# Kernel optimization log

Hardware: AMD Instinct MI355X
Metric: run time of the kernel (lower is better)

The kernel has to match this reference:

```python
import jax, jax.numpy as jnp
import numpy as np

B, H, W = 4, 180, 180
C_L, C_C, C_OUT = 128, 128, 256
CH_ALL = 2 * (C_L + C_C)        # 512
CH_HID = CH_ALL // 3            # 170


def setup_inputs() -> dict:
    key = jax.random.key(0)
    ks = jax.random.split(key, 12)
    N = 160000
    inp = {
        'lidar_features': jax.random.normal(ks[0], (N, C_L), dtype=jnp.float32),
        'img_bev': jax.random.normal(ks[1], (B, C_C, H, W), dtype=jnp.float32),
        'batch_idx': jnp.sort(jax.random.randint(ks[2], (N,), 0, B, dtype=jnp.int32)),
        'y_idx': jax.random.randint(ks[3], (N,), 0, H, dtype=jnp.int32),
        'x_idx': jax.random.randint(ks[4], (N,), 0, W, dtype=jnp.int32),
        # weights stored as [in, out] (x @ W), equivalent to torch Linear weight.T
        'Wl1': jax.random.normal(ks[5], (CH_ALL, CH_HID), dtype=jnp.float32) * 0.02,
        'Wl2': jax.random.normal(ks[6], (CH_HID, C_L), dtype=jnp.float32) * 0.02,
        'Wc1': jax.random.normal(ks[7], (CH_ALL, CH_HID), dtype=jnp.float32) * 0.02,
        'Wc2': jax.random.normal(ks[8], (CH_HID, C_C), dtype=jnp.float32) * 0.02,
        'Wf1': jax.random.normal(ks[9], (C_L + C_C, C_OUT), dtype=jnp.float32) * 0.02,
        'Wf2': jax.random.normal(ks[10], (C_OUT, C_OUT), dtype=jnp.float32) * 0.02,
    }
    return inp


def reference(lidar_features, img_bev, Wl1, Wl2, Wc1, Wc2, Wf1, Wf2,
              batch_idx, y_idx, x_idx):
    relu = jax.nn.relu
    spatial_size = H * W
    # flatten dense image BEV map: [B,C,H,W] -> [B*H*W, C]
    img_flat = jnp.transpose(img_bev, (0, 2, 3, 1)).reshape(B * H * W, C_C)
    # per-voxel flat row index (faithful to original incl. clamp to spatial_size-2)
    row = batch_idx * spatial_size + y_idx * W + x_idx
    row = jnp.clip(row, 0, spatial_size - 2)
    cam_feat = img_flat[row]                                  # [N, C_C] gather
    # per-batch segment min/max (ragged reduction)
    lmin = jax.ops.segment_min(lidar_features, batch_idx, num_segments=B)
    lmax = jax.ops.segment_max(lidar_features, batch_idx, num_segments=B)
    cmin = jax.ops.segment_min(cam_feat, batch_idx, num_segments=B)
    cmax = jax.ops.segment_max(cam_feat, batch_idx, num_segments=B)
    cat_mm = jnp.concatenate([lmin, lmax, cmin, cmax], axis=-1)   # [B, 512]
    att_l = jax.nn.sigmoid(relu(relu(cat_mm @ Wl1) @ Wl2))        # [B, C_L]
    att_c = jax.nn.sigmoid(relu(relu(cat_mm @ Wc1) @ Wc2))        # [B, C_C]
    gated_l = lidar_features * att_l[batch_idx]
    gated_c = cam_feat * att_c[batch_idx]
    fused = jnp.concatenate([gated_l, gated_c], axis=-1)          # [N, 256]
    out = relu(relu(fused @ Wf1) @ Wf2)                           # [N, 256]
    return out
```

## Files before the change

kernel.cpp:

```cpp
#include <hip/hip_runtime.h>
#include <math.h>

#define NB 4
#define HH 180
#define WWW 180
#define SPATIAL (HH*WWW)
#define CH_HID 170
#define CLAMP_ROW (SPATIAL-2)
#define SLAB 8192
#define CHUNKB 256

typedef short v8s __attribute__((ext_vector_type(8)));
typedef short v4s __attribute__((ext_vector_type(4)));
typedef float v4f __attribute__((ext_vector_type(4)));

__device__ __forceinline__ unsigned short f2bf(float f) {
    unsigned u = __float_as_uint(f);
    u += 0x7FFFu + ((u >> 16) & 1);
    return (unsigned short)(u >> 16);
}
__device__ __forceinline__ v4f vmin4(v4f a, v4f b) {
    v4f r; r[0]=fminf(a[0],b[0]); r[1]=fminf(a[1],b[1]); r[2]=fminf(a[2],b[2]); r[3]=fminf(a[3],b[3]); return r;
}
__device__ __forceinline__ v4f vmax4(v4f a, v4f b) {
    v4f r; r[0]=fmaxf(a[0],b[0]); r[1]=fmaxf(a[1],b[1]); r[2]=fmaxf(a[2],b[2]); r[3]=fmaxf(a[3],b[3]); return r;
}

__global__ void k_prep(const float* __restrict__ Wf1, const float* __restrict__ Wf2,
                       unsigned short* __restrict__ W1S, unsigned short* __restrict__ W2S) {
    const float* W = blockIdx.y ? Wf2 : Wf1;
    unsigned short* WS = blockIdx.y ? W2S : W1S;
    const int tid = threadIdx.x;
    const int frag = blockIdx.x * 4 + (tid >> 6);
    const int lane = tid & 63;
    const int nt = frag >> 3, ks = frag & 7;
    const int q = lane >> 4, ml = lane & 15;
    v8s pk;
    #pragma unroll
    for (int j = 0; j < 8; ++j)
        pk[j] = (short)f2bf(W[(ks*32 + q*8 + j)*256 + nt*16 + ml]);
    *(v8s*)&WS[(frag*64 + lane)*8] = pk;
}

__global__ void k_setup(const float* __restrict__ img, float* __restrict__ camT) {
    __shared__ float tile[32][33];
    int s0 = blockIdx.x * 32, c0 = blockIdx.y * 32;
    int lx = threadIdx.x & 31, ly = threadIdx.x >> 5;
    for (int i = 0; i < 4; ++i) {
        int s = s0 + lx;
        if (s < SPATIAL)
            tile[ly + i*8][lx] = img[(c0 + ly + i*8) * SPATIAL + s];
    }
    __syncthreads();
    for (int i = 0; i < 4; ++i) {
        int s = s0 + ly + i*8;
        if (s < SPATIAL)
            camT[s*128 + c0 + lx] = tile[lx][ly + i*8];
    }
}

__global__ __launch_bounds__(256)
void k_reduce(const float* __restrict__ lidar, const float* __restrict__ camT,
              const int* __restrict__ bidx, const int* __restrict__ yidx,
              const int* __restrict__ xidx,
              float* __restrict__ pA, float* __restrict__ pB, int N, int nblkA) {
    __shared__ __align__(16) char sm[32768];
    const int tid = threadIdx.x;

    if ((int)blockIdx.x < nblkA) {
        v4f (*red)[8][32] = (v4f(*)[8][32])sm;
        const int total = N * 32;
        const int beg = blockIdx.x * SLAB;
        const int end = min(beg + SLAB, total);
        const v4f pinf = {INFINITY, INFINITY, INFINITY, INFINITY};
        const v4f ninf = {-INFINITY, -INFINITY, -INFINITY, -INFINITY};
        v4f mn0 = pinf, mn1 = pinf, mn2 = pinf, mn3 = pinf;
        v4f mx0 = ninf, mx1 = ninf, mx2 = ninf, mx3 = ninf;

        #define ACCUM(vv, bb) do { \
            bool m0_ = ((bb) == 0), m1_ = ((bb) == 1), m2_ = ((bb) == 2), m3_ = ((bb) == 3); \
            mn0 = m0_ ? vmin4(mn0, (vv)) : mn0;  mx0 = m0_ ? vmax4(mx0, (vv)) : mx0; \
            mn1 = m1_ ? vmin4(mn1, (vv)) : mn1;  mx1 = m1_ ? vmax4(mx1, (vv)) : mx1; \
            mn2 = m2_ ? vmin4(mn2, (vv)) : mn2;  mx2 = m2_ ? vmax4(mx2, (vv)) : mx2; \
            mn3 = m3_ ? vmin4(mn3, (vv)) : mn3;  mx3 = m3_ ? vmax4(mx3, (vv)) : mx3; \
        } while (0)

        int i = beg + tid;
        for (; i + 768 < end; i += 1024) {
            v4f x0 = *(const v4f*)&lidar[(size_t)i * 4];
            v4f x1 = *(const v4f*)&lidar[(size_t)(i + 256) * 4];
            v4f x2 = *(const v4f*)&lidar[(size_t)(i + 512) * 4];
            v4f x3 = *(const v4f*)&lidar[(size_t)(i + 768) * 4];
            int b0 = bidx[i >> 5];
            int b1 = bidx[(i + 256) >> 5];
            int b2 = bidx[(i + 512) >> 5];
            int b3 = bidx[(i + 768) >> 5];
            ACCUM(x0, b0); ACCUM(x1, b1); ACCUM(x2, b2); ACCUM(x3, b3);
        }
        for (; i < end; i += 256) {
            v4f x = *(const v4f*)&lidar[(size_t)i * 4];
            int b = bidx[i >> 5];
            ACCUM(x, b);
        }
        #undef ACCUM

        const int sub = tid >> 5, cc = tid & 31;
        red[sub][0][cc] = mn0; red[sub][1][cc] = mx0;
        red[sub][2][cc] = mn1; red[sub][3][cc] = mx1;
        red[sub][4][cc] = mn2; red[sub][5][cc] = mx2;
        red[sub][6][cc] = mn3; red[sub][7][cc] = mx3;
        __syncthreads();
        const int acc = tid >> 5;
        const bool ismax = acc & 1;
        v4f r = red[0][acc][cc];
        #pragma unroll
        for (int s = 1; s < 8; ++s)
            r = ismax ? vmax4(r, red[s][acc][cc]) : vmin4(r, red[s][acc][cc]);
        *(v4f*)&pA[((size_t)blockIdx.x * 8 + acc) * 128 + cc * 4] = r;
    } else {
        int* srow = (int*)sm;
        v4f (*cred)[2][32] = (v4f(*)[2][32])(sm + 2048);
        const int blk = blockIdx.x - nblkA;
        const int vbeg = blk * CHUNKB;
        const int cnt = min(CHUNKB, N - vbeg);
        const bool active = (cnt > 0) && (bidx[vbeg] == 0);
        if (!active) {
            int a2 = tid >> 7, ch = tid & 127;
            pB[((size_t)blk * 2 + a2) * 128 + ch] = a2 ? -INFINITY : INFINITY;
            return;
        }
        if (tid < cnt) {
            int v = vbeg + tid;
            srow[tid] = (bidx[v] == 0) ? min(yidx[v] * WWW + xidx[v], CLAMP_ROW) : -1;
        }
        __syncthreads();
        const int c4 = (tid & 31) * 4;
        v4f mn = {INFINITY, INFINITY, INFINITY, INFINITY};
        v4f mx = {-INFINITY, -INFINITY, -INFINITY, -INFINITY};
        for (int idx = tid >> 5; idx < cnt; idx += 8) {
            int r = srow[idx];
            if (r >= 0) {
                v4f v = *(const v4f*)&camT[(size_t)r * 128 + c4];
                mn = vmin4(mn, v);
                mx = vmax4(mx, v);
            }
        }
        const int sub = tid >> 5, cc = tid & 31;
        cred[sub][0][cc] = mn;
        cred[sub][1][cc] = mx;
        __syncthreads();
        if (tid < 64) {
            const bool ismax = tid >= 32;
            v4f r = cred[0][ismax][cc];
            #pragma unroll
            for (int s = 1; s < 8; ++s)
                r = ismax ? vmax4(r, cred[s][ismax][cc]) : vmin4(r, cred[s][ismax][cc]);
            *(v4f*)&pB[((size_t)blk * 2 + (ismax ? 1 : 0)) * 128 + cc * 4] = r;
        }
    }
}

__global__ __launch_bounds__(256)
void k_fin(const float* __restrict__ pA, const float* __restrict__ pB,
           float* __restrict__ statsf, int nblkA, int nblkB) {
    __shared__ float red2[8][33];
    const int bx = blockIdx.x, tid = threadIdx.x;
    const int g = tid >> 5, l = tid & 31;
    const bool iscam = bx >= 32;
    const int acc = iscam ? ((bx - 32) >> 2) : (bx >> 2);
    const int quarter = bx & 3;
    const int ch = quarter * 32 + l;
    const int nrow = iscam ? nblkB : nblkA;
    const bool ismax = iscam ? (acc == 1) : ((acc & 1) != 0);
    const float* base = iscam ? (pB + acc * 128 + ch) : (pA + acc * 128 + ch);
    const size_t rstride = iscam ? 256 : 1024;

    float r = ismax ? -INFINITY : INFINITY;
    int row = g;
    for (; row + 24 < nrow; row += 32) {
        float a = base[(size_t)row * rstride];
        float b = base[(size_t)(row + 8) * rstride];
        float c = base[(size_t)(row + 16) * rstride];
        float d = base[(size_t)(row + 24) * rstride];
        if (ismax) r = fmaxf(fmaxf(r, a), fmaxf(fmaxf(b, c), d));
        else       r = fminf(fminf(r, a), fminf(fminf(b, c), d));
    }
    for (; row < nrow; row += 8) {
        float a = base[(size_t)row * rstride];
        r = ismax ? fmaxf(r, a) : fminf(r, a);
    }
    red2[g][l] = r;
    __syncthreads();
    if (tid < 32) {
        float v = red2[0][l];
        #pragma unroll
        for (int s = 1; s < 8; ++s)
            v = ismax ? fmaxf(v, red2[s][l]) : fminf(v, red2[s][l]);
        int off;
        if (iscam) off = 256 + acc * 128 + ch;
        else { int bb = acc >> 1; off = bb * 512 + (acc & 1) * 128 + ch; }
        statsf[off] = v;
    }
}

__global__ void k_mlp(const float* __restrict__ statsf, const float* __restrict__ camT,
                      const float* __restrict__ Wl1, const float* __restrict__ Wl2,
                      const float* __restrict__ Wc1, const float* __restrict__ Wc2,
                      float* __restrict__ att) {
    __shared__ float cat[512];
    __shared__ float hid[CH_HID];
    int b = blockIdx.x >> 1;
    int net = blockIdx.x & 1;
    const float* W1 = net ? Wc1 : Wl1;
    const float* W2 = net ? Wc2 : Wl2;
    int tid = threadIdx.x;
    for (int j = tid; j < 512; j += 256) {
        float x;
        if (j < 256 || b == 0) x = statsf[b * 512 + j];
        else                   x = camT[(size_t)CLAMP_ROW * 128 + (j & 127)];
        cat[j] = x;
    }
    __syncthreads();
    if (tid < CH_HID) {
        float s = 0.f;
        #pragma unroll 16
        for (int k = 0; k < 512; ++k) s += cat[k] * W1[k*CH_HID + tid];
        hid[tid] = fmaxf(s, 0.f);
    }
    __syncthreads();
    if (tid < 128) {
        float s = 0.f;
        #pragma unroll 10
        for (int k = 0; k < CH_HID; ++k) s += hid[k] * W2[k*128 + tid];
        s = fmaxf(s, 0.f);
        att[b*256 + net*128 + tid] = 1.f / (1.f + expf(-s));
    }
}

__global__ __launch_bounds__(256, 4)
void k_main(const float* __restrict__ lidar, const float* __restrict__ camT,
            const int* __restrict__ bidx, const int* __restrict__ yidx,
            const int* __restrict__ xidx, const float* __restrict__ att,
            const unsigned short* __restrict__ W1S, const unsigned short* __restrict__ W2S,
            float* __restrict__ out, int N) {
    __shared__ __align__(16) char smem[64 * 264 * 2];
    unsigned short (*sA)[264] = (unsigned short(*)[264])smem;
    float* sAf = (float*)smem;
    __shared__ int srow[64];
    __shared__ int sbb[64];
    const int tid = threadIdx.x;
    const int v0 = blockIdx.x * 64;

    if (tid < 64) {
        int v = v0 + tid;
        int b = 0, row = 0;
        if (v < N) {
            b = bidx[v];
            row = min(b*SPATIAL + yidx[v]*WWW + xidx[v], CLAMP_ROW);
        }
        sbb[tid] = b;
        srow[tid] = row;
    }
    const int c = (tid & 63) * 4;
    const bool cam = (c >= 128);
    v4f attv0 = *(const v4f*)&att[0*256 + c];
    v4f attv1 = *(const v4f*)&att[1*256 + c];
    v4f attv2 = *(const v4f*)&att[2*256 + c];
    v4f attv3 = *(const v4f*)&att[3*256 + c];
    __syncthreads();

    #pragma unroll
    for (int half = 0; half < 2; ++half) {
        v4f x[8]; int bm[8];
        #pragma unroll
        for (int j = 0; j < 8; ++j) {
            int m = (half*8 + j)*4 + (tid >> 6);
            int vc = min(v0 + m, N - 1);
            bm[j] = sbb[m];
            const float* src = cam ? &camT[(size_t)srow[m]*128 + (c - 128)]
                                   : &lidar[(size_t)vc*128 + c];
            x[j] = *(const v4f*)src;
        }
        #pragma unroll
        for (int j = 0; j < 8; ++j) {
            int m = (half*8 + j)*4 + (tid >> 6);
            int b = bm[j];
            v4f a = attv0;
            if (b == 1) a = attv1;
            if (b == 2) a = attv2;
            if (b == 3) a = attv3;
            v4f val = x[j] * a;
            v4s pk;
            #pragma unroll
            for (int jj = 0; jj < 4; ++jj) pk[jj] = (short)f2bf(val[jj]);
            *(v4s*)&sA[m][c] = pk;
        }
    }

    const int wave = tid >> 6;
    const int lane = tid & 63;
    const int ml = lane & 15;
    const int q = lane >> 4;

    v4f acc[4][4];
    for (int layer = 0; layer < 2; ++layer) {
        const unsigned short* WS = layer ? W2S : W1S;
        const v4f zz = {0.f, 0.f, 0.f, 0.f};
        for (int rt = 0; rt < 4; ++rt)
            for (int ct = 0; ct < 4; ++ct) acc[rt][ct] = zz;

        __syncthreads();
        #pragma unroll
        for (int ks = 0; ks < 8; ++ks) {
            v8s a[4];
            const int ka = ks*32 + q*8;
            #pragma unroll
            for (int rt = 0; rt < 4; ++rt)
                a[rt] = *(const v8s*)&sA[rt*16 + ml][ka];
            #pragma unroll
            for (int ct = 0; ct < 4; ++ct) {
                v8s bfr = *(const v8s*)&WS[(((wave*4 + ct)*8 + ks)*64 + lane)*8];
                #pragma unroll
                for (int rt = 0; rt < 4; ++rt)
                    acc[rt][ct] = __builtin_amdgcn_mfma_f32_16x16x32_bf16(
                        a[rt], bfr, acc[rt][ct], 0, 0, 0);
            }
        }
        __syncthreads();
        if (layer == 0) {
            for (int rt = 0; rt < 4; ++rt)
                for (int ct = 0; ct < 4; ++ct)
                    for (int r = 0; r < 4; ++r)
                        sA[rt*16 + q*4 + r][wave*64 + ct*16 + ml] =
                            f2bf(fmaxf(acc[rt][ct][r], 0.f));
        }
    }

    const int c4 = (tid & 63) * 4;
    #pragma unroll
    for (int p = 0; p < 2; ++p) {
        __syncthreads();
        #pragma unroll
        for (int rt = 2*p; rt < 2*p + 2; ++rt)
            for (int ct = 0; ct < 4; ++ct)
                for (int r = 0; r < 4; ++r)
                    sAf[((rt - 2*p)*16 + q*4 + r)*260 + wave*64 + ct*16 + ml] =
                        fmaxf(acc[rt][ct][r], 0.f);
        __syncthreads();
        #pragma unroll
        for (int i = 0; i < 8; ++i) {
            int rl = (tid >> 6) + i*4;
            int v = v0 + p*32 + rl;
            if (v < N)
                *(v4f*)&out[(size_t)v*256 + c4] = *(const v4f*)&sAf[rl*260 + c4];
        }
    }
}

extern "C" void kernel_launch(void* const* d_in, const int* in_sizes, int n_in,
                              void* d_out, int out_size, void* d_ws, size_t ws_size,
                              hipStream_t stream) {
    const float* lidar = (const float*)d_in[0];
    const float* img   = (const float*)d_in[1];
    const int*   bidx  = (const int*)d_in[2];
    const int*   yidx  = (const int*)d_in[3];
    const int*   xidx  = (const int*)d_in[4];
    const float* Wl1   = (const float*)d_in[5];
    const float* Wl2   = (const float*)d_in[6];
    const float* Wc1   = (const float*)d_in[7];
    const float* Wc2   = (const float*)d_in[8];
    const float* Wf1   = (const float*)d_in[9];
    const float* Wf2   = (const float*)d_in[10];
    float* out = (float*)d_out;
    const int N = in_sizes[0] / 128;

    float* statsf = (float*)d_ws;
    float* att = (float*)((char*)d_ws + 8192);
    unsigned short* W1S = (unsigned short*)((char*)d_ws + 16384);
    unsigned short* W2S = (unsigned short*)((char*)d_ws + 16384 + 131072);
    float* camT = (float*)((char*)d_ws + 16384 + 262144);

    const int nblkA = (N * 32 + SLAB - 1) / SLAB;
    const int nblkB = (N + CHUNKB - 1) / CHUNKB;
    const size_t pA_bytes = (size_t)nblkA * 8 * 128 * 4;
    const size_t pB_bytes = (size_t)nblkB * 2 * 128 * 4;
    const size_t pA_off = 16384 + 262144 + (size_t)SPATIAL * 128 * 4;
    float *pA, *pB;
    if (ws_size >= pA_off + pA_bytes + pB_bytes) {
        pA = (float*)((char*)d_ws + pA_off);
    } else {
        size_t off = ((size_t)out_size - (pA_bytes + pB_bytes)) & ~(size_t)255;
        pA = (float*)((char*)out + off);
    }
    pB = (float*)((char*)pA + pA_bytes);

    k_prep<<<dim3(32, 2), 256, 0, stream>>>(Wf1, Wf2, W1S, W2S);
    k_setup<<<dim3((SPATIAL + 31) / 32, 4), 256, 0, stream>>>(img, camT);
    k_reduce<<<nblkA + nblkB, 256, 0, stream>>>(lidar, camT, bidx, yidx, xidx, pA, pB, N, nblkA);
    k_fin<<<40, 256, 0, stream>>>(pA, pB, statsf, nblkA, nblkB);
    k_mlp<<<8, 256, 0, stream>>>(statsf, camT, Wl1, Wl2, Wc1, Wc2, att);
    k_main<<<(N + 63) / 64, 256, 0, stream>>>(lidar, camT, bidx, yidx, xidx, att, W1S, W2S, out, N);
}
```

Baseline: 393.2 us.

## Merge prep, transpose and lidar reduce into fewer launches; fold cam finalize into MLP

Weight packing, the image transpose and the lidar min/max reduction now run as one launch. The camera gather reduction and the lidar finalize share a second launch, and the camera min/max finalize moves into the attention MLP kernel. Camera chunk size is halved so that reduction spreads over more blocks. k_main's launch bounds drop from 4 to 3 blocks per SM. This cuts launch count and idle gaps between small kernels, at the cost of serial partial reduction inside k_mlp and possibly lower occupancy in k_main.

Result: slower. 458.6 us (+16.6%).

```diff
diff --git a/kernel.cpp b/kernel.cpp
--- a/kernel.cpp
+++ b/kernel.cpp
@@ -8,7 +8,7 @@
 #define CH_HID 170
 #define CLAMP_ROW (SPATIAL-2)
 #define SLAB 8192
-#define CHUNKB 256
+#define CHUNKB 128
 
 typedef short v8s __attribute__((ext_vector_type(8)));
 typedef short v4s __attribute__((ext_vector_type(4)));
@@ -26,51 +26,51 @@
     v4f r; r[0]=fmaxf(a[0],b[0]); r[1]=fmaxf(a[1],b[1]); r[2]=fmaxf(a[2],b[2]); r[3]=fmaxf(a[3],b[3]); return r;
 }
 
-__global__ void k_prep(const float* __restrict__ Wf1, const float* __restrict__ Wf2,
-                       unsigned short* __restrict__ W1S, unsigned short* __restrict__ W2S) {
-    const float* W = blockIdx.y ? Wf2 : Wf1;
-    unsigned short* WS = blockIdx.y ? W2S : W1S;
-    const int tid = threadIdx.x;
-    const int frag = blockIdx.x * 4 + (tid >> 6);
-    const int lane = tid & 63;
-    const int nt = frag >> 3, ks = frag & 7;
-    const int q = lane >> 4, ml = lane & 15;
-    v8s pk;
-    #pragma unroll
-    for (int j = 0; j < 8; ++j)
-        pk[j] = (short)f2bf(W[(ks*32 + q*8 + j)*256 + nt*16 + ml]);
-    *(v8s*)&WS[(frag*64 + lane)*8] = pk;
-}
-
-__global__ void k_setup(const float* __restrict__ img, float* __restrict__ camT) {
-    __shared__ float tile[32][33];
-    int s0 = blockIdx.x * 32, c0 = blockIdx.y * 32;
-    int lx = threadIdx.x & 31, ly = threadIdx.x >> 5;
-    for (int i = 0; i < 4; ++i) {
-        int s = s0 + lx;
-        if (s < SPATIAL)
-            tile[ly + i*8][lx] = img[(c0 + ly + i*8) * SPATIAL + s];
-    }
-    __syncthreads();
-    for (int i = 0; i < 4; ++i) {
-        int s = s0 + ly + i*8;
-        if (s < SPATIAL)
-            camT[s*128 + c0 + lx] = tile[lx][ly + i*8];
-    }
-}
-
 __global__ __launch_bounds__(256)
-void k_reduce(const float* __restrict__ lidar, const float* __restrict__ camT,
-              const int* __restrict__ bidx, const int* __restrict__ yidx,
-              const int* __restrict__ xidx,
-              float* __restrict__ pA, float* __restrict__ pB, int N, int nblkA) {
+void k1(const float* __restrict__ Wf1, const float* __restrict__ Wf2,
+        unsigned short* __restrict__ W1S, unsigned short* __restrict__ W2S,
+        const float* __restrict__ img, float* __restrict__ camT,
+        const float* __restrict__ lidar, const int* __restrict__ bidx,
+        float* __restrict__ pA, int N, int nsetup, int nblkA) {
     __shared__ __align__(16) char sm[32768];
     const int tid = threadIdx.x;
-
-    if ((int)blockIdx.x < nblkA) {
+    const int bx = blockIdx.x;
+
+    if (bx < 64) {
+        const int net = bx >> 5, xb = bx & 31;
+        const float* W = net ? Wf2 : Wf1;
+        unsigned short* WS = net ? W2S : W1S;
+        const int frag = xb * 4 + (tid >> 6);
+        const int lane = tid & 63;
+        const int nt = frag >> 3, ks = frag & 7;
+        const int q = lane >> 4, ml = lane & 15;
+        v8s pk;
+        #pragma unroll
+        for (int j = 0; j < 8; ++j)
+            pk[j] = (short)f2bf(W[(ks*32 + q*8 + j)*256 + nt*16 + ml]);
+        *(v8s*)&WS[(frag*64 + lane)*8] = pk;
+    } else if (bx < 64 + nsetup) {
+        float (*tile)[33] = (float(*)[33])sm;
+        const int bs = bx - 64;
+        const int sx = bs % 1013, sy = bs / 1013;
+        int s0 = sx * 32, c0 = sy * 32;
+        int lx = tid & 31, ly = tid >> 5;
+        for (int i = 0; i < 4; ++i) {
+            int s = s0 + lx;
+            if (s < SPATIAL)
+                tile[ly + i*8][lx] = img[(c0 + ly + i*8) * SPATIAL + s];
+        }
+        __syncthreads();
+        for (int i = 0; i < 4; ++i) {
+            int s = s0 + ly + i*8;
+            if (s < SPATIAL)
+                camT[s*128 + c0 + lx] = tile[lx][ly + i*8];
+        }
+    } else {
         v4f (*red)[8][32] = (v4f(*)[8][32])sm;
+        const int ba = bx - 64 - nsetup;
         const int total = N * 32;
-        const int beg = blockIdx.x * SLAB;
+        const int beg = ba * SLAB;
         const int end = min(beg + SLAB, total);
         const v4f pinf = {INFINITY, INFINITY, INFINITY, INFINITY};
         const v4f ninf = {-INFINITY, -INFINITY, -INFINITY, -INFINITY};
@@ -116,17 +116,29 @@
         #pragma unroll
         for (int s = 1; s < 8; ++s)
             r = ismax ? vmax4(r, red[s][acc][cc]) : vmin4(r, red[s][acc][cc]);
-        *(v4f*)&pA[((size_t)blockIdx.x * 8 + acc) * 128 + cc * 4] = r;
-    } else {
+        *(v4f*)&pA[((size_t)ba * 8 + acc) * 128 + cc * 4] = r;
+    }
+}
+
+__global__ __launch_bounds__(256)
+void k2(const float* __restrict__ camT,
+        const int* __restrict__ bidx, const int* __restrict__ yidx,
+        const int* __restrict__ xidx,
+        const float* __restrict__ pA, float* __restrict__ pB,
+        float* __restrict__ statsf, int N, int nblkA, int nblkB) {
+    __shared__ __align__(16) char sm[12288];
+    const int tid = threadIdx.x;
+    const int bx = blockIdx.x;
+
+    if (bx < nblkB) {
         int* srow = (int*)sm;
         v4f (*cred)[2][32] = (v4f(*)[2][32])(sm + 2048);
-        const int blk = blockIdx.x - nblkA;
-        const int vbeg = blk * CHUNKB;
+        const int vbeg = bx * CHUNKB;
         const int cnt = min(CHUNKB, N - vbeg);
         const bool active = (cnt > 0) && (bidx[vbeg] == 0);
         if (!active) {
             int a2 = tid >> 7, ch = tid & 127;
-            pB[((size_t)blk * 2 + a2) * 128 + ch] = a2 ? -INFINITY : INFINITY;
+            pB[((size_t)bx * 2 + a2) * 128 + ch] = a2 ? -INFINITY : INFINITY;
             return;
         }
         if (tid < cnt) {
@@ -155,58 +167,50 @@
             #pragma unroll
             for (int s = 1; s < 8; ++s)
                 r = ismax ? vmax4(r, cred[s][ismax][cc]) : vmin4(r, cred[s][ismax][cc]);
-            *(v4f*)&pB[((size_t)blk * 2 + (ismax ? 1 : 0)) * 128 + cc * 4] = r;
-        }
-    }
-}
-
-__global__ __launch_bounds__(256)
-void k_fin(const float* __restrict__ pA, const float* __restrict__ pB,
-           float* __restrict__ statsf, int nblkA, int nblkB) {
-    __shared__ float red2[8][33];
-    const int bx = blockIdx.x, tid = threadIdx.x;
-    const int g = tid >> 5, l = tid & 31;
-    const bool iscam = bx >= 32;
-    const int acc = iscam ? ((bx - 32) >> 2) : (bx >> 2);
-    const int quarter = bx & 3;
-    const int ch = quarter * 32 + l;
-    const int nrow = iscam ? nblkB : nblkA;
-    const bool ismax = iscam ? (acc == 1) : ((acc & 1) != 0);
-    const float* base = iscam ? (pB + acc * 128 + ch) : (pA + acc * 128 + ch);
-    const size_t rstride = iscam ? 256 : 1024;
-
-    float r = ismax ? -INFINITY : INFINITY;
-    int row = g;
-    for (; row + 24 < nrow; row += 32) {
-        float a = base[(size_t)row * rstride];
-        float b = base[(size_t)(row + 8) * rstride];
-        float c = base[(size_t)(row + 16) * rstride];
-        float d = base[(size_t)(row + 24) * rstride];
-        if (ismax) r = fmaxf(fmaxf(r, a), fmaxf(fmaxf(b, c), d));
-        else       r = fminf(fminf(r, a), fminf(fminf(b, c), d));
-    }
-    for (; row < nrow; row += 8) {
-        float a = base[(size_t)row * rstride];
-        r = ismax ? fmaxf(r, a) : fminf(r, a);
-    }
-    red2[g][l] = r;
-    __syncthreads();
-    if (tid < 32) {
-        float v = red2[0][l];
-        #pragma unroll
-        for (int s = 1; s < 8; ++s)
-            v = ismax ? fmaxf(v, red2[s][l]) : fminf(v, red2[s][l]);
-        int off;
-        if (iscam) off = 256 + acc * 128 + ch;
-        else { int bb = acc >> 1; off = bb * 512 + (acc & 1) * 128 + ch; }
-        statsf[off] = v;
-    }
-}
-
-__global__ void k_mlp(const float* __restrict__ statsf, const float* __restrict__ camT,
+            *(v4f*)&pB[((size_t)bx * 2 + (ismax ? 1 : 0)) * 128 + cc * 4] = r;
+        }
+    } else {
+        float (*red2)[33] = (float(*)[33])sm;
+        const int bf = bx - nblkB;
+        const int g = tid >> 5, l = tid & 31;
+        const int acc = bf >> 2;
+        const int quarter = bf & 3;
+        const int ch = quarter * 32 + l;
+        const bool ismax = (acc & 1) != 0;
+        const float* base = pA + acc * 128 + ch;
+
+        float r = ismax ? -INFINITY : INFINITY;
+        int row = g;
+        for (; row + 24 < nblkA; row += 32) {
+            float a = base[(size_t)row * 1024];
+            float b = base[(size_t)(row + 8) * 1024];
+            float c = base[(size_t)(row + 16) * 1024];
+            float d = base[(size_t)(row + 24) * 1024];
+            if (ismax) r = fmaxf(fmaxf(r, a), fmaxf(fmaxf(b, c), d));
+            else       r = fminf(fminf(r, a), fminf(fminf(b, c), d));
+        }
+        for (; row < nblkA; row += 8) {
+            float a = base[(size_t)row * 1024];
+            r = ismax ? fmaxf(r, a) : fminf(r, a);
+        }
+        red2[g][l] = r;
+        __syncthreads();
+        if (tid < 32) {
+            float v = red2[0][l];
+            #pragma unroll
+            for (int s = 1; s < 8; ++s)
+                v = ismax ? fmaxf(v, red2[s][l]) : fminf(v, red2[s][l]);
+            int bb = acc >> 1;
+            statsf[bb * 512 + (acc & 1) * 128 + ch] = v;
+        }
+    }
+}
+
+__global__ void k_mlp(const float* __restrict__ statsf, const float* __restrict__ pB,
+                      const float* __restrict__ camT,
                       const float* __restrict__ Wl1, const float* __restrict__ Wl2,
                       const float* __restrict__ Wc1, const float* __restrict__ Wc2,
-                      float* __restrict__ att) {
+                      float* __restrict__ att, int nblkB) {
     __shared__ float cat[512];
     __shared__ float hid[CH_HID];
     int b = blockIdx.x >> 1;
@@ -216,8 +220,30 @@
     int tid = threadIdx.x;
     for (int j = tid; j < 512; j += 256) {
         float x;
-        if (j < 256 || b == 0) x = statsf[b * 512 + j];
-        else                   x = camT[(size_t)CLAMP_ROW * 128 + (j & 127)];
+        if (j < 256) {
+            x = statsf[b * 512 + j];
+        } else if (b == 0) {
+            const bool ismax = (j >= 384);
+            const int ch = j & 127;
+            const float* base = pB + (ismax ? 128 : 0) + ch;
+            float r = ismax ? -INFINITY : INFINITY;
+            int row = 0;
+            for (; row + 3 < nblkB; row += 4) {
+                float a = base[(size_t)row * 256];
+                float c1 = base[(size_t)(row + 1) * 256];
+                float c2 = base[(size_t)(row + 2) * 256];
+                float c3 = base[(size_t)(row + 3) * 256];
+                if (ismax) r = fmaxf(fmaxf(r, a), fmaxf(fmaxf(c1, c2), c3));
+                else       r = fminf(fminf(r, a), fminf(fminf(c1, c2), c3));
+            }
+            for (; row < nblkB; ++row) {
+                float a = base[(size_t)row * 256];
+                r = ismax ? fmaxf(r, a) : fminf(r, a);
+            }
+            x = r;
+        } else {
+            x = camT[(size_t)CLAMP_ROW * 128 + (j & 127)];
+        }
         cat[j] = x;
     }
     __syncthreads();
@@ -237,7 +263,7 @@
     }
 }
 
-__global__ __launch_bounds__(256, 4)
+__global__ __launch_bounds__(256, 3)
 void k_main(const float* __restrict__ lidar, const float* __restrict__ camT,
             const int* __restrict__ bidx, const int* __restrict__ yidx,
             const int* __restrict__ xidx, const float* __restrict__ att,
@@ -380,6 +406,7 @@
     unsigned short* W2S = (unsigned short*)((char*)d_ws + 16384 + 131072);
     float* camT = (float*)((char*)d_ws + 16384 + 262144);
 
+    const int nsetup = ((SPATIAL + 31) / 32) * 4;
     const int nblkA = (N * 32 + SLAB - 1) / SLAB;
     const int nblkB = (N + CHUNKB - 1) / CHUNKB;
     const size_t pA_bytes = (size_t)nblkA * 8 * 128 * 4;
@@ -394,10 +421,9 @@
     }
     pB = (float*)((char*)pA + pA_bytes);
 
-    k_prep<<<dim3(32, 2), 256, 0, stream>>>(Wf1, Wf2, W1S, W2S);
-    k_setup<<<dim3((SPATIAL + 31) / 32, 4), 256, 0, stream>>>(img, camT);
-    k_reduce<<<nblkA + nblkB, 256, 0, stream>>>(lidar, camT, bidx, yidx, xidx, pA, pB, N, nblkA);
-    k_fin<<<40, 256, 0, stream>>>(pA, pB, statsf, nblkA, nblkB);
-    k_mlp<<<8, 256, 0, stream>>>(statsf, camT, Wl1, Wl2, Wc1, Wc2, att);
+    k1<<<64 + nsetup + nblkA, 256, 0, stream>>>(Wf1, Wf2, W1S, W2S, img, camT,
+                                                lidar, bidx, pA, N, nsetup, nblkA);
+    k2<<<nblkB + 32, 256, 0, stream>>>(camT, bidx, yidx, xidx, pA, pB, statsf, N, nblkA, nblkB);
+    k_mlp<<<8, 256, 0, stream>>>(statsf, pB, camT, Wl1, Wl2, Wc1, Wc2, att, nblkB);
     k_main<<<(N + 63) / 64, 256, 0, stream>>>(lidar, camT, bidx, yidx, xidx, att, W1S, W2S, out, N);
 }
```
